# Performance work log

Hardware: AMD Instinct MI355X
Metric: run time of the kernel (lower is better)

## Reference

```python
import jax, jax.numpy as jnp
import numpy as np

B, N, D, H, M, NN, K = 2, 2048, 256, 8, 2, 2048, 8


def setup_inputs() -> dict:
    key = jax.random.key(0)
    ks = jax.random.split(key, 8)
    s = 0.02
    return {
        "current_points": jax.random.normal(ks[0], (B, N, 3), jnp.float32),
        "current_features": jax.random.normal(ks[1], (B, N, D), jnp.float32),
        "neighbor_points": jax.random.normal(ks[2], (M, B, NN, 3), jnp.float32),
        "neighbor_features": jax.random.normal(ks[3], (M, B, NN, D), jnp.float32),
        "in_proj_w": jax.random.normal(ks[4], (3 * D, D), jnp.float32) * s,
        "in_proj_b": jnp.zeros((3 * D,), jnp.float32),
        "out_proj_w": jax.random.normal(ks[5], (D, D), jnp.float32) * s,
        "out_proj_b": jnp.zeros((D,), jnp.float32),
        "spatial_w": jax.random.normal(ks[6], (D, 3), jnp.float32) * s,
        "spatial_b": jnp.zeros((D,), jnp.float32),
    }


def _knn_edge_features(points, features, k):
    # points [b,n,3], features [b,n,d] -> edge features [b,n,d]
    sq = jnp.sum(points * points, axis=-1)                       # [b,n]
    d2 = sq[:, :, None] + sq[:, None, :] - 2.0 * jnp.einsum('bnc,bmc->bnm', points, points)
    _, idx = jax.lax.top_k(-d2, k)                               # k nearest (incl. self), [b,n,k]
    b_idx = jnp.arange(points.shape[0])[:, None, None]
    nbr = features[b_idx, idx]                                   # gather neighbor feats [b,n,k,d]
    return features - jnp.mean(nbr, axis=2)


def _mha(q, kv, in_w, in_b, out_w, out_b, h):
    # torch nn.MultiheadAttention (batch_first) cross-attention
    d = q.shape[-1]
    dh = d // h
    wq, wk, wv = jnp.split(in_w, 3, axis=0)
    bq, bk, bv = jnp.split(in_b, 3, axis=0)
    qp = q @ wq.T + bq                                           # [b,Lq,d]
    kp = kv @ wk.T + bk                                          # [b,Lk,d]
    vp = kv @ wv.T + bv

    def heads(x):
        b, l, _ = x.shape
        return x.reshape(b, l, h, dh).transpose(0, 2, 1, 3)      # [b,h,l,dh]

    qh, kh, vh = heads(qp), heads(kp), heads(vp)
    scores = jnp.einsum('bhqd,bhkd->bhqk', qh, kh) / np.sqrt(dh).astype(np.float32)
    attn = jax.nn.softmax(scores, axis=-1)
    o = jnp.einsum('bhqk,bhkd->bhqd', attn, vh)
    b, _, lq, _ = o.shape
    o = o.transpose(0, 2, 1, 3).reshape(b, lq, d)
    return o @ out_w.T + out_b


def reference(current_points, current_features, neighbor_points, neighbor_features,
              in_proj_w, in_proj_b, out_proj_w, out_proj_b, spatial_w, spatial_b):
    cur_edge = _knn_edge_features(current_points, current_features, K)       # [B,N,D]
    nbr_edge = jax.vmap(lambda p, f: _knn_edge_features(p, f, K))(neighbor_points, neighbor_features)  # [M,B,NN,D]
    all_nbr = jnp.transpose(nbr_edge, (1, 0, 2, 3)).reshape(B, M * NN, D)    # cat along seq dim
    aligned = _mha(cur_edge, all_nbr, in_proj_w, in_proj_b, out_proj_w, out_proj_b, H)
    spatial = current_points @ spatial_w.T + spatial_b                       # [B,N,D]
    return aligned + spatial
```

## Files before the change

kernel.cpp:

```cpp
#include <hip/hip_runtime.h>
#include <hip/hip_bf16.h>

typedef __bf16 bf16_t;
typedef __attribute__((ext_vector_type(8))) __bf16 bf16x8;
typedef __attribute__((ext_vector_type(4))) __bf16 bf16x4;
typedef __attribute__((ext_vector_type(4))) float f32x4;


__global__ __launch_bounds__(256) void wconv_kernel(const float* __restrict__ w_in,
                                                    const float* __restrict__ w_out,
                                                    bf16_t* __restrict__ w_in_b,
                                                    bf16_t* __restrict__ w_out_b) {
    int i = blockIdx.x * 256 + threadIdx.x;
    if (i < 768 * 256) w_in_b[i] = (bf16_t)w_in[i];
    if (i < 256 * 256) w_out_b[i] = (bf16_t)w_out[i];
}

__global__ __launch_bounds__(1024) void knn_kernel(const float* __restrict__ cur_pts,
                                                   const float* __restrict__ nbr_pts,
                                                   int* __restrict__ idx_out) {
    int p = blockIdx.y;
    const float* pts = (p < 2) ? (cur_pts + (size_t)p * 2048 * 3)
                               : (nbr_pts + (size_t)(p - 2) * 2048 * 3);

    __shared__ __align__(16) float4 spts[2048];

    int tid = threadIdx.x;
    for (int i = tid; i < 2048; i += 1024) {
        float x = pts[i * 3 + 0], y = pts[i * 3 + 1], z = pts[i * 3 + 2];
        float sq = __fadd_rn(__fadd_rn(__fmul_rn(x, x), __fmul_rn(y, y)), __fmul_rn(z, z));
        spts[i] = make_float4(x, y, z, sq);
    }
    __syncthreads();

    int wave = tid >> 6, lane = tid & 63;
    int q = blockIdx.x * 16 + wave;
    float4 qp4 = spts[q];

    float dist[8];
    int di[8];
#pragma unroll
    for (int r = 0; r < 8; r++) { dist[r] = 3.4e38f; di[r] = 0x7fffffff; }

    for (int t = 0; t < 32; t++) {
        int j = t * 64 + lane;
        float4 pp = spts[j];
        float dot = __fadd_rn(__fadd_rn(__fmul_rn(qp4.x, pp.x), __fmul_rn(qp4.y, pp.y)),
                              __fmul_rn(qp4.z, pp.z));
        float d2 = __fsub_rn(__fadd_rn(qp4.w, pp.w), __fmul_rn(2.0f, dot));
        if (d2 < dist[7]) {
#pragma unroll
            for (int r = 7; r >= 1; --r) {
                bool cm = d2 < dist[r - 1];
                bool cr = d2 < dist[r];
                float nd = cm ? dist[r - 1] : (cr ? d2 : dist[r]);
                int ni = cm ? di[r - 1] : (cr ? j : di[r]);
                dist[r] = nd; di[r] = ni;
            }
            if (d2 < dist[0]) { dist[0] = d2; di[0] = j; }
        }
    }

    int res[8];
#pragma unroll
    for (int r = 0; r < 8; r++) {
        float bd = dist[0];
        int bi = di[0];
#pragma unroll
        for (int m = 1; m < 64; m <<= 1) {
            float od = __shfl_xor(bd, m);
            int oi = __shfl_xor(bi, m);
            if (od < bd || (od == bd && oi < bi)) { bd = od; bi = oi; }
        }
        res[r] = bi;
        bool win = (di[0] == bi);
#pragma unroll
        for (int k = 0; k < 7; k++) {
            dist[k] = win ? dist[k + 1] : dist[k];
            di[k]   = win ? di[k + 1]   : di[k];
        }
        if (win) { dist[7] = 3.4e38f; di[7] = 0x7fffffff; }
    }

    if (lane == 0) {
        int4* o = (int4*)(idx_out + ((size_t)p * 2048 + q) * 8);
        o[0] = make_int4(res[0], res[1], res[2], res[3]);
        o[1] = make_int4(res[4], res[5], res[6], res[7]);
    }
}

__global__ __launch_bounds__(64) void edge_kernel(const float* __restrict__ cur_feat,
                                                  const float* __restrict__ nbr_feat,
                                                  const int* __restrict__ idx_buf,
                                                  bf16_t* __restrict__ cur_edge,
                                                  bf16_t* __restrict__ all_nbr) {
    int blk = blockIdx.x;
    int p = blk >> 11, q = blk & 2047;
    const float* feat;
    bf16_t* outp;
    if (p < 2) {
        feat = cur_feat + (size_t)p * 2048 * 256;
        outp = cur_edge + ((size_t)p * 2048 + q) * 256;
    } else {
        int mb = p - 2;
        int m = mb >> 1, bb = mb & 1;
        feat = nbr_feat + (size_t)mb * 2048 * 256;
        outp = all_nbr + ((size_t)bb * 4096 + m * 2048 + q) * 256;
    }
    const int* idx = idx_buf + ((size_t)p * 2048 + q) * 8;
    int t = threadIdx.x;
    float4 self = ((const float4*)(feat + (size_t)q * 256))[t];
    float sx = 0.f, sy = 0.f, sz = 0.f, sw = 0.f;
#pragma unroll
    for (int r = 0; r < 8; r++) {
        float4 f = ((const float4*)(feat + (size_t)idx[r] * 256))[t];
        sx += f.x; sy += f.y; sz += f.z; sw += f.w;
    }
    bf16x4 v;
    v[0] = (bf16_t)(self.x - sx * 0.125f);
    v[1] = (bf16_t)(self.y - sy * 0.125f);
    v[2] = (bf16_t)(self.z - sz * 0.125f);
    v[3] = (bf16_t)(self.w - sw * 0.125f);
    *(bf16x4*)(outp + 4 * t) = v;
}

__global__ __launch_bounds__(256) void qkv_kernel(const bf16_t* __restrict__ cur_edge,
                                                  const bf16_t* __restrict__ all_nbr,
                                                  const bf16_t* __restrict__ w_in,
                                                  const float* __restrict__ b_in,
                                                  bf16_t* __restrict__ qp,
                                                  bf16_t* __restrict__ kp,
                                                  bf16_t* __restrict__ vpT) {
    int z = blockIdx.z;
    int Mrows = (z == 0) ? 4096 : 8192;
    int m0base = blockIdx.y * 64;
    if (m0base >= Mrows) return;
    const bf16_t* A = (z == 0) ? cur_edge : all_nbr;
    const bf16_t* W = w_in + (size_t)z * 256 * 256;

    int wave = threadIdx.x >> 6, lane = threadIdx.x & 63;
    int wr = wave >> 1, wc = wave & 1;
    int m0 = m0base + wr * 32;
    int n0 = blockIdx.x * 64 + wc * 32;
    int lr = lane & 15, lg = lane >> 4;

    f32x4 acc[2][2] = {};
    for (int kc = 0; kc < 256; kc += 32) {
        bf16x8 a[2], b[2];
#pragma unroll
        for (int i = 0; i < 2; i++)
            a[i] = *(const bf16x8*)(A + (size_t)(m0 + i * 16 + lr) * 256 + kc + lg * 8);
#pragma unroll
        for (int i = 0; i < 2; i++)
            b[i] = *(const bf16x8*)(W + (size_t)(n0 + i * 16 + lr) * 256 + kc + lg * 8);
#pragma unroll
        for (int i = 0; i < 2; i++)
#pragma unroll
            for (int j = 0; j < 2; j++)
                acc[i][j] = __builtin_amdgcn_mfma_f32_16x16x32_bf16(a[i], b[j], acc[i][j], 0, 0, 0);
    }

    const float inv_s = 0.17677669529663687f;
#pragma unroll
    for (int i = 0; i < 2; i++)
#pragma unroll
        for (int j = 0; j < 2; j++)
#pragma unroll
            for (int r = 0; r < 4; r++) {
                int mm = m0 + i * 16 + lg * 4 + r;
                int nn = n0 + j * 16 + lr;
                float v = acc[i][j][r] + b_in[z * 256 + nn];
                if (z == 0) {
                    qp[(size_t)mm * 256 + nn] = (bf16_t)(v * inv_s);
                } else if (z == 1) {
                    kp[(size_t)mm * 256 + nn] = (bf16_t)v;
                } else {
                    int bb = mm >> 12, kv = mm & 4095, h = nn >> 5, dd = nn & 31;
                    vpT[(((size_t)bb * 8 + h) * 32 + dd) * 4096 + kv] = (bf16_t)v;
                }
            }
}

__global__ __launch_bounds__(256) void attn_kernel(const bf16_t* __restrict__ qp,
                                                   const bf16_t* __restrict__ kp,
                                                   const bf16_t* __restrict__ vpT,
                                                   bf16_t* __restrict__ Opart,
                                                   float* __restrict__ Lpart) {
    int bh = blockIdx.y;
    int b = bh >> 3, h = bh & 7;
    int c = blockIdx.z;
    int wave = threadIdx.x >> 6, lane = threadIdx.x & 63;
    int lr = lane & 15, lg = lane >> 4;
    int q0 = blockIdx.x * 128 + wave * 32;

    const bf16_t* Qb = qp + ((size_t)b * 2048 + q0) * 256 + h * 32;
    const bf16_t* Kb = kp + (size_t)b * 4096 * 256 + h * 32;
    const bf16_t* Vb = vpT + ((size_t)b * 8 + h) * 32 * 4096;

    __shared__ __align__(16) bf16_t P_lds[4][2][16][32];

    bf16x8 qfrag[2];
    qfrag[0] = *(const bf16x8*)(Qb + (size_t)lr * 256 + lg * 8);
    qfrag[1] = *(const bf16x8*)(Qb + (size_t)(16 + lr) * 256 + lg * 8);

    f32x4 oacc[2][2] = {};
    float lsum[2][4] = {};
    const f32x4 zf = {0.f, 0.f, 0.f, 0.f};

    int kv_lo = c * 1024, kv_hi = kv_lo + 1024;
    for (int kv0 = kv_lo; kv0 < kv_hi; kv0 += 32) {
        bf16x8 kfrag[2];
        kfrag[0] = *(const bf16x8*)(Kb + (size_t)(kv0 + lr) * 256 + lg * 8);
        kfrag[1] = *(const bf16x8*)(Kb + (size_t)(kv0 + 16 + lr) * 256 + lg * 8);

#pragma unroll
        for (int ms = 0; ms < 2; ms++) {
            f32x4 s0 = __builtin_amdgcn_mfma_f32_16x16x32_bf16(qfrag[ms], kfrag[0], zf, 0, 0, 0);
            f32x4 s1 = __builtin_amdgcn_mfma_f32_16x16x32_bf16(qfrag[ms], kfrag[1], zf, 0, 0, 0);
#pragma unroll
            for (int r = 0; r < 4; r++) {
                float p0 = __expf(s0[r]);
                float p1 = __expf(s1[r]);
                lsum[ms][r] += p0 + p1;
                P_lds[wave][ms][lg * 4 + r][lr] = (bf16_t)p0;
                P_lds[wave][ms][lg * 4 + r][16 + lr] = (bf16_t)p1;
            }
        }

        bf16x8 vfrag[2];
        vfrag[0] = *(const bf16x8*)(Vb + (size_t)lr * 4096 + kv0 + lg * 8);
        vfrag[1] = *(const bf16x8*)(Vb + (size_t)(16 + lr) * 4096 + kv0 + lg * 8);

#pragma unroll
        for (int ms = 0; ms < 2; ms++) {
            bf16x8 pf = *(const bf16x8*)(&P_lds[wave][ms][lr][lg * 8]);
            oacc[ms][0] = __builtin_amdgcn_mfma_f32_16x16x32_bf16(pf, vfrag[0], oacc[ms][0], 0, 0, 0);
            oacc[ms][1] = __builtin_amdgcn_mfma_f32_16x16x32_bf16(pf, vfrag[1], oacc[ms][1], 0, 0, 0);
        }
    }

#pragma unroll
    for (int ms = 0; ms < 2; ms++)
#pragma unroll
        for (int r = 0; r < 4; r++) {
            float s = lsum[ms][r];
            s += __shfl_xor(s, 1);
            s += __shfl_xor(s, 2);
            s += __shfl_xor(s, 4);
            s += __shfl_xor(s, 8);
            lsum[ms][r] = s;
        }

#pragma unroll
    for (int ms = 0; ms < 2; ms++)
#pragma unroll
        for (int r = 0; r < 4; r++) {
            int qq = q0 + ms * 16 + lg * 4 + r;
            if (lr == 0)
                Lpart[(((size_t)c * 2 + b) * 8 + h) * 2048 + qq] = lsum[ms][r];
#pragma unroll
            for (int ds = 0; ds < 2; ds++) {
                int dd = h * 32 + ds * 16 + lr;
                Opart[(((size_t)c * 2 + b) * 2048 + qq) * 256 + dd] = (bf16_t)oacc[ms][ds][r];
            }
        }
}

__global__ __launch_bounds__(256) void attn_combine(const bf16_t* __restrict__ Opart,
                                                    const float* __restrict__ Lpart,
                                                    bf16_t* __restrict__ o_buf) {
    int t = blockIdx.x * 256 + threadIdx.x;
    int row = t >> 5;
    int c8 = (t & 31) * 8;
    int b = row >> 11, q = row & 2047, h = c8 >> 5;

    float acc[8] = {};
    float l = 0.f;
#pragma unroll
    for (int c = 0; c < 4; c++) {
        bf16x8 v = *(const bf16x8*)(Opart + (((size_t)c * 2 + b) * 2048 + q) * 256 + c8);
#pragma unroll
        for (int j = 0; j < 8; j++) acc[j] += (float)v[j];
        l += Lpart[(((size_t)c * 2 + b) * 8 + h) * 2048 + q];
    }
    float rl = 1.0f / l;
    bf16x8 o;
#pragma unroll
    for (int j = 0; j < 8; j++) o[j] = (bf16_t)(acc[j] * rl);
    *(bf16x8*)(o_buf + (size_t)row * 256 + c8) = o;
}

__global__ __launch_bounds__(256) void outproj_kernel(const bf16_t* __restrict__ o_buf,
                                                      const bf16_t* __restrict__ w_out,
                                                      const float* __restrict__ b_out,
                                                      const float* __restrict__ cur_pts,
                                                      const float* __restrict__ sw,
                                                      const float* __restrict__ sb,
                                                      float* __restrict__ out) {
    int wave = threadIdx.x >> 6, lane = threadIdx.x & 63;
    int wr = wave >> 1, wc = wave & 1;
    int m0 = blockIdx.y * 64 + wr * 32;
    int n0 = blockIdx.x * 64 + wc * 32;
    int lr = lane & 15, lg = lane >> 4;

    f32x4 acc[2][2] = {};
    for (int kc = 0; kc < 256; kc += 32) {
        bf16x8 a[2], b[2];
#pragma unroll
        for (int i = 0; i < 2; i++)
            a[i] = *(const bf16x8*)(o_buf + (size_t)(m0 + i * 16 + lr) * 256 + kc + lg * 8);
#pragma unroll
        for (int i = 0; i < 2; i++)
            b[i] = *(const bf16x8*)(w_out + (size_t)(n0 + i * 16 + lr) * 256 + kc + lg * 8);
#pragma unroll
        for (int i = 0; i < 2; i++)
#pragma unroll
            for (int j = 0; j < 2; j++)
                acc[i][j] = __builtin_amdgcn_mfma_f32_16x16x32_bf16(a[i], b[j], acc[i][j], 0, 0, 0);
    }

#pragma unroll
    for (int i = 0; i < 2; i++)
#pragma unroll
        for (int j = 0; j < 2; j++)
#pragma unroll
            for (int r = 0; r < 4; r++) {
                int mm = m0 + i * 16 + lg * 4 + r;
                int nn = n0 + j * 16 + lr;
                const float* pp = cur_pts + (size_t)mm * 3;
                float sp = pp[0] * sw[nn * 3 + 0] + pp[1] * sw[nn * 3 + 1] + pp[2] * sw[nn * 3 + 2] + sb[nn];
                out[(size_t)mm * 256 + nn] = acc[i][j][r] + b_out[nn] + sp;
            }
}

extern "C" void kernel_launch(void* const* d_in, const int* in_sizes, int n_in,
                              void* d_out, int out_size, void* d_ws, size_t ws_size,
                              hipStream_t stream) {
    const float* cur_pts  = (const float*)d_in[0];
    const float* cur_feat = (const float*)d_in[1];
    const float* nbr_pts  = (const float*)d_in[2];
    const float* nbr_feat = (const float*)d_in[3];
    const float* in_w     = (const float*)d_in[4];
    const float* in_b     = (const float*)d_in[5];
    const float* out_w    = (const float*)d_in[6];
    const float* out_b    = (const float*)d_in[7];
    const float* sw       = (const float*)d_in[8];
    const float* sb       = (const float*)d_in[9];

    char* ws = (char*)d_ws;
    bf16_t* w_in_b  = (bf16_t*)(ws + 0);
    bf16_t* w_out_b = (bf16_t*)(ws + 393216);
    int*    idx_buf = (int*)(ws + 524288);
    bf16_t* cur_edge = (bf16_t*)(ws + 917504);
    bf16_t* all_nbr  = (bf16_t*)(ws + 3014656);
    bf16_t* qp  = (bf16_t*)(ws + 7208960);
    bf16_t* kp  = (bf16_t*)(ws + 9306112);
    bf16_t* vpT = (bf16_t*)(ws + 13500416);
    bf16_t* o_buf = (bf16_t*)(ws + 17694720);
    bf16_t* Opart = (bf16_t*)(ws + 19791872);
    float*  Lpart = (float*)(ws + 28180480);
    float* outp = (float*)d_out;

    wconv_kernel<<<dim3(768), dim3(256), 0, stream>>>(in_w, out_w, w_in_b, w_out_b);
    knn_kernel<<<dim3(128, 6), dim3(1024), 0, stream>>>(cur_pts, nbr_pts, idx_buf);
    edge_kernel<<<dim3(12288), dim3(64), 0, stream>>>(cur_feat, nbr_feat, idx_buf, cur_edge, all_nbr);
    qkv_kernel<<<dim3(4, 128, 3), dim3(256), 0, stream>>>(cur_edge, all_nbr, w_in_b, in_b, qp, kp, vpT);
    attn_kernel<<<dim3(16, 16, 4), dim3(256), 0, stream>>>(qp, kp, vpT, Opart, Lpart);
    attn_combine<<<dim3(512), dim3(256), 0, stream>>>(Opart, Lpart, o_buf);
    outproj_kernel<<<dim3(4, 64), dim3(256), 0, stream>>>(o_buf, w_out_b, out_b, cur_pts, sw, sb, outp);
}
```

Baseline: 221.3 us.

## Stage K/V tiles cooperatively in LDS and halve queries per wave in attention

The attention kernel now has each wave handle 16 query rows instead of 32, and the grid is doubled to cover them. K and V tiles for each 32-key step are loaded once per block by the four waves, each wave loading one quarter, and held in shared memory with a register prefetch of the next tile. Previously every wave fetched its own K/V fragments from global memory. The change cuts redundant global loads and raises occupancy (launch bounds 256,8), but adds two block barriers per iteration and halves MFMA work per wave, so latency hiding depends on having many resident blocks.

```diff
diff --git a/kernel.cpp b/kernel.cpp
--- a/kernel.cpp
+++ b/kernel.cpp
@@ -181,89 +181,101 @@
             }
 }
 
-__global__ __launch_bounds__(256) void attn_kernel(const bf16_t* __restrict__ qp,
-                                                   const bf16_t* __restrict__ kp,
-                                                   const bf16_t* __restrict__ vpT,
-                                                   bf16_t* __restrict__ Opart,
-                                                   float* __restrict__ Lpart) {
+__global__ __launch_bounds__(256, 8) void attn_kernel(const bf16_t* __restrict__ qp,
+                                                      const bf16_t* __restrict__ kp,
+                                                      const bf16_t* __restrict__ vpT,
+                                                      bf16_t* __restrict__ Opart,
+                                                      float* __restrict__ Lpart) {
     int bh = blockIdx.y;
     int b = bh >> 3, h = bh & 7;
     int c = blockIdx.z;
     int wave = threadIdx.x >> 6, lane = threadIdx.x & 63;
     int lr = lane & 15, lg = lane >> 4;
-    int q0 = blockIdx.x * 128 + wave * 32;
+    int q0 = blockIdx.x * 64 + wave * 16;
 
     const bf16_t* Qb = qp + ((size_t)b * 2048 + q0) * 256 + h * 32;
     const bf16_t* Kb = kp + (size_t)b * 4096 * 256 + h * 32;
     const bf16_t* Vb = vpT + ((size_t)b * 8 + h) * 32 * 4096;
 
-    __shared__ __align__(16) bf16_t P_lds[4][2][16][32];
-
-    bf16x8 qfrag[2];
-    qfrag[0] = *(const bf16x8*)(Qb + (size_t)lr * 256 + lg * 8);
-    qfrag[1] = *(const bf16x8*)(Qb + (size_t)(16 + lr) * 256 + lg * 8);
-
-    f32x4 oacc[2][2] = {};
-    float lsum[2][4] = {};
+    __shared__ __align__(16) bf16_t KV[2048];
+    __shared__ __align__(16) bf16_t P_lds[4][512];
+    bf16_t* Pw = &P_lds[wave][0];
+
+    bf16x8 qfrag = *(const bf16x8*)(Qb + (size_t)lr * 256 + lg * 8);
+
+    f32x4 oacc[2] = {};
+    float lsum[4] = {};
     const f32x4 zf = {0.f, 0.f, 0.f, 0.f};
 
-    int kv_lo = c * 1024, kv_hi = kv_lo + 1024;
-    for (int kv0 = kv_lo; kv0 < kv_hi; kv0 += 32) {
-        bf16x8 kfrag[2];
-        kfrag[0] = *(const bf16x8*)(Kb + (size_t)(kv0 + lr) * 256 + lg * 8);
-        kfrag[1] = *(const bf16x8*)(Kb + (size_t)(kv0 + 16 + lr) * 256 + lg * 8);
-
-#pragma unroll
-        for (int ms = 0; ms < 2; ms++) {
-            f32x4 s0 = __builtin_amdgcn_mfma_f32_16x16x32_bf16(qfrag[ms], kfrag[0], zf, 0, 0, 0);
-            f32x4 s1 = __builtin_amdgcn_mfma_f32_16x16x32_bf16(qfrag[ms], kfrag[1], zf, 0, 0, 0);
-#pragma unroll
-            for (int r = 0; r < 4; r++) {
-                float p0 = __expf(s0[r]);
-                float p1 = __expf(s1[r]);
-                lsum[ms][r] += p0 + p1;
-                P_lds[wave][ms][lg * 4 + r][lr] = (bf16_t)p0;
-                P_lds[wave][ms][lg * 4 + r][16 + lr] = (bf16_t)p1;
-            }
-        }
-
-        bf16x8 vfrag[2];
-        vfrag[0] = *(const bf16x8*)(Vb + (size_t)lr * 4096 + kv0 + lg * 8);
-        vfrag[1] = *(const bf16x8*)(Vb + (size_t)(16 + lr) * 4096 + kv0 + lg * 8);
-
-#pragma unroll
-        for (int ms = 0; ms < 2; ms++) {
-            bf16x8 pf = *(const bf16x8*)(&P_lds[wave][ms][lr][lg * 8]);
-            oacc[ms][0] = __builtin_amdgcn_mfma_f32_16x16x32_bf16(pf, vfrag[0], oacc[ms][0], 0, 0, 0);
-            oacc[ms][1] = __builtin_amdgcn_mfma_f32_16x16x32_bf16(pf, vfrag[1], oacc[ms][1], 0, 0, 0);
-        }
-    }
-
-#pragma unroll
-    for (int ms = 0; ms < 2; ms++)
+    int kv_lo = c * 1024;
+
+    int role = wave;
+    int tlr = lr, tlg = lg;
+    const bf16_t* gsrc;
+    size_t gstep;
+    if (role < 2) {
+        gsrc = Kb + (size_t)(kv_lo + role * 16 + tlr) * 256 + tlg * 8;
+        gstep = 32 * 256;
+    } else {
+        gsrc = Vb + (size_t)((role - 2) * 16 + tlr) * 4096 + kv_lo + tlg * 8;
+        gstep = 32;
+    }
+    bf16_t* stage_dst = &KV[(size_t)threadIdx.x * 8];
+
+    bf16x8 g = *(const bf16x8*)gsrc;
+    gsrc += gstep;
+
+    for (int t = 0; t < 32; t++) {
+        *(bf16x8*)stage_dst = g;
+        if (t + 1 < 32) {
+            g = *(const bf16x8*)gsrc;
+            gsrc += gstep;
+        }
+        __syncthreads();
+
+        bf16x8 kf0 = *(const bf16x8*)(KV + (size_t)lane * 8);
+        bf16x8 kf1 = *(const bf16x8*)(KV + 512 + (size_t)lane * 8);
+        bf16x8 vf0 = *(const bf16x8*)(KV + 1024 + (size_t)lane * 8);
+        bf16x8 vf1 = *(const bf16x8*)(KV + 1536 + (size_t)lane * 8);
+
+        f32x4 s0 = __builtin_amdgcn_mfma_f32_16x16x32_bf16(qfrag, kf0, zf, 0, 0, 0);
+        f32x4 s1 = __builtin_amdgcn_mfma_f32_16x16x32_bf16(qfrag, kf1, zf, 0, 0, 0);
 #pragma unroll
         for (int r = 0; r < 4; r++) {
-            float s = lsum[ms][r];
-            s += __shfl_xor(s, 1);
-            s += __shfl_xor(s, 2);
-            s += __shfl_xor(s, 4);
-            s += __shfl_xor(s, 8);
-            lsum[ms][r] = s;
-        }
-
-#pragma unroll
-    for (int ms = 0; ms < 2; ms++)
-#pragma unroll
-        for (int r = 0; r < 4; r++) {
-            int qq = q0 + ms * 16 + lg * 4 + r;
-            if (lr == 0)
-                Lpart[(((size_t)c * 2 + b) * 8 + h) * 2048 + qq] = lsum[ms][r];
-#pragma unroll
-            for (int ds = 0; ds < 2; ds++) {
-                int dd = h * 32 + ds * 16 + lr;
-                Opart[(((size_t)c * 2 + b) * 2048 + qq) * 256 + dd] = (bf16_t)oacc[ms][ds][r];
-            }
-        }
+            float p0 = __expf(s0[r]);
+            float p1 = __expf(s1[r]);
+            lsum[r] += p0 + p1;
+            Pw[((lr >> 3) * 128) + (lg * 4 + r) * 8 + (lr & 7)] = (bf16_t)p0;
+            Pw[((2 + (lr >> 3)) * 128) + (lg * 4 + r) * 8 + (lr & 7)] = (bf16_t)p1;
+        }
+        bf16x8 pf = *(const bf16x8*)(Pw + (size_t)lane * 8);
+        oacc[0] = __builtin_amdgcn_mfma_f32_16x16x32_bf16(pf, vf0, oacc[0], 0, 0, 0);
+        oacc[1] = __builtin_amdgcn_mfma_f32_16x16x32_bf16(pf, vf1, oacc[1], 0, 0, 0);
+
+        __syncthreads();
+    }
+
+#pragma unroll
+    for (int r = 0; r < 4; r++) {
+        float s = lsum[r];
+        s += __shfl_xor(s, 1);
+        s += __shfl_xor(s, 2);
+        s += __shfl_xor(s, 4);
+        s += __shfl_xor(s, 8);
+        lsum[r] = s;
+    }
+
+#pragma unroll
+    for (int r = 0; r < 4; r++) {
+        int qq = q0 + lg * 4 + r;
+        if (lr == 0)
+            Lpart[(((size_t)c * 2 + b) * 8 + h) * 2048 + qq] = lsum[r];
+#pragma unroll
+        for (int ds = 0; ds < 2; ds++) {
+            int dd = h * 32 + ds * 16 + lr;
+            Opart[(((size_t)c * 2 + b) * 2048 + qq) * 256 + dd] = (bf16_t)oacc[ds][r];
+        }
+    }
 }
 
 __global__ __launch_bounds__(256) void attn_combine(const bf16_t* __restrict__ Opart,
@@ -365,7 +377,7 @@
     knn_kernel<<<dim3(128, 6), dim3(1024), 0, stream>>>(cur_pts, nbr_pts, idx_buf);
     edge_kernel<<<dim3(12288), dim3(64), 0, stream>>>(cur_feat, nbr_feat, idx_buf, cur_edge, all_nbr);
     qkv_kernel<<<dim3(4, 128, 3), dim3(256), 0, stream>>>(cur_edge, all_nbr, w_in_b, in_b, qp, kp, vpT);
-    attn_kernel<<<dim3(16, 16, 4), dim3(256), 0, stream>>>(qp, kp, vpT, Opart, Lpart);
+    attn_kernel<<<dim3(32, 16, 4), dim3(256), 0, stream>>>(qp, kp, vpT, Opart, Lpart);
     attn_combine<<<dim3(512), dim3(256), 0, stream>>>(Opart, Lpart, o_buf);
     outproj_kernel<<<dim3(4, 64), dim3(256), 0, stream>>>(o_buf, w_out_b, out_b, cur_pts, sw, sb, outp);
 }
```

New measurement: 202.6 us. 8.5% less time.

## Transpose V via LDS, swizzle P tile, remap attention blocks for XCD locality

Applied to the files above, without the earlier changes.

The QKV projection now writes V row-major, and a new transpose kernel builds the per-head V^T through shared memory. This replaces the scattered strided stores in the QKV epilogue. The attention kernel swaps MFMA operands so each lane holds consecutive kv scores, packs P into 8-byte LDS stores with an XOR swizzle, and reduces row sums with fewer shuffles. It also loads K and V fragments together up front, flattens the grid with a mapping that puts the same head and chunk on one XCD, and sets occupancy launch bounds. The cost is one extra kernel launch and an extra V round trip through memory, with the vp buffer aliased over the Opart region.

```diff
diff --git a/kernel.cpp b/kernel.cpp
--- a/kernel.cpp
+++ b/kernel.cpp
@@ -6,6 +6,12 @@
 typedef __attribute__((ext_vector_type(4))) __bf16 bf16x4;
 typedef __attribute__((ext_vector_type(4))) float f32x4;
 
+
+static __device__ __forceinline__ unsigned pk2(float x, float y) {
+    unsigned short ux = __builtin_bit_cast(unsigned short, (bf16_t)x);
+    unsigned short uy = __builtin_bit_cast(unsigned short, (bf16_t)y);
+    return (unsigned)ux | ((unsigned)uy << 16);
+}
 
 __global__ __launch_bounds__(256) void wconv_kernel(const float* __restrict__ w_in,
                                                     const float* __restrict__ w_out,
@@ -130,7 +136,7 @@
                                                   const float* __restrict__ b_in,
                                                   bf16_t* __restrict__ qp,
                                                   bf16_t* __restrict__ kp,
-                                                  bf16_t* __restrict__ vpT) {
+                                                  bf16_t* __restrict__ vp) {
     int z = blockIdx.z;
     int Mrows = (z == 0) ? 4096 : 8192;
     int m0base = blockIdx.y * 64;
@@ -175,89 +181,133 @@
                 } else if (z == 1) {
                     kp[(size_t)mm * 256 + nn] = (bf16_t)v;
                 } else {
-                    int bb = mm >> 12, kv = mm & 4095, h = nn >> 5, dd = nn & 31;
-                    vpT[(((size_t)bb * 8 + h) * 32 + dd) * 4096 + kv] = (bf16_t)v;
+                    vp[(size_t)mm * 256 + nn] = (bf16_t)v;
                 }
             }
 }
 
-__global__ __launch_bounds__(256) void attn_kernel(const bf16_t* __restrict__ qp,
-                                                   const bf16_t* __restrict__ kp,
-                                                   const bf16_t* __restrict__ vpT,
-                                                   bf16_t* __restrict__ Opart,
-                                                   float* __restrict__ Lpart) {
+__global__ __launch_bounds__(256) void vt_kernel(const bf16_t* __restrict__ vp,
+                                                 bf16_t* __restrict__ vpT) {
+    int kc = blockIdx.x;
     int bh = blockIdx.y;
     int b = bh >> 3, h = bh & 7;
-    int c = blockIdx.z;
+    __shared__ bf16_t tile[64][34];
+    int tid = threadIdx.x;
+
+    const bf16_t* src = vp + ((size_t)b * 4096 + kc * 64) * 256 + h * 32;
+    int dd0 = (tid & 7) * 4, kvr = tid >> 3;
+#pragma unroll
+    for (int it = 0; it < 2; it++) {
+        int kv = it * 32 + kvr;
+        bf16x4 v = *(const bf16x4*)(src + (size_t)kv * 256 + dd0);
+#pragma unroll
+        for (int j = 0; j < 4; j++) tile[kv][dd0 + j] = v[j];
+    }
+    __syncthreads();
+
+    bf16_t* dst = vpT + (((size_t)b * 8 + h) * 32) * 4096 + kc * 64;
+    int kv0 = (tid & 15) * 4, ddr0 = tid >> 4;
+#pragma unroll
+    for (int it = 0; it < 2; it++) {
+        int dd = it * 16 + ddr0;
+        bf16x4 v;
+#pragma unroll
+        for (int j = 0; j < 4; j++) v[j] = tile[kv0 + j][dd];
+        *(bf16x4*)(dst + (size_t)dd * 4096 + kv0) = v;
+    }
+}
+
+__global__ __launch_bounds__(256, 4) void attn_kernel(const bf16_t* __restrict__ qp,
+                                                      const bf16_t* __restrict__ kp,
+                                                      const bf16_t* __restrict__ vpT,
+                                                      bf16_t* __restrict__ Opart,
+                                                      float* __restrict__ Lpart) {
+    int d = blockIdx.x;
+    int xcd = d & 7, j = d >> 3;
+    int xb = j & 15;
+    int g = xcd + 8 * (j >> 4);
+    int bh = g & 15, c = g >> 4;
+    int b = bh >> 3, h = bh & 7;
+
     int wave = threadIdx.x >> 6, lane = threadIdx.x & 63;
     int lr = lane & 15, lg = lane >> 4;
-    int q0 = blockIdx.x * 128 + wave * 32;
+    int q0 = xb * 128 + wave * 32;
 
     const bf16_t* Qb = qp + ((size_t)b * 2048 + q0) * 256 + h * 32;
     const bf16_t* Kb = kp + (size_t)b * 4096 * 256 + h * 32;
     const bf16_t* Vb = vpT + ((size_t)b * 8 + h) * 32 * 4096;
 
-    __shared__ __align__(16) bf16_t P_lds[4][2][16][32];
-
-    bf16x8 qfrag[2];
-    qfrag[0] = *(const bf16x8*)(Qb + (size_t)lr * 256 + lg * 8);
-    qfrag[1] = *(const bf16x8*)(Qb + (size_t)(16 + lr) * 256 + lg * 8);
+    __shared__ __align__(16) char P_lds[4][2048];
+    char* Pw = &P_lds[wave][0];
+
+    bf16x8 qf[2];
+    qf[0] = *(const bf16x8*)(Qb + (size_t)lr * 256 + lg * 8);
+    qf[1] = *(const bf16x8*)(Qb + (size_t)(16 + lr) * 256 + lg * 8);
 
     f32x4 oacc[2][2] = {};
-    float lsum[2][4] = {};
+    float lsum[2] = {0.f, 0.f};
     const f32x4 zf = {0.f, 0.f, 0.f, 0.f};
 
-    int kv_lo = c * 1024, kv_hi = kv_lo + 1024;
-    for (int kv0 = kv_lo; kv0 < kv_hi; kv0 += 32) {
-        bf16x8 kfrag[2];
-        kfrag[0] = *(const bf16x8*)(Kb + (size_t)(kv0 + lr) * 256 + lg * 8);
-        kfrag[1] = *(const bf16x8*)(Kb + (size_t)(kv0 + 16 + lr) * 256 + lg * 8);
+    int wb[2][2], rb[2];
+#pragma unroll
+    for (int ms = 0; ms < 2; ms++) {
+        rb[ms] = (ms * 16 + lr) * 64 + ((lg ^ (lr & 3)) << 4);
+#pragma unroll
+        for (int kvs = 0; kvs < 2; kvs++)
+            wb[ms][kvs] = (ms * 16 + lr) * 64 +
+                          (((kvs * 2 + (lg >> 1)) ^ (lr & 3)) << 4) + ((lg & 1) << 3);
+    }
+
+    int kv_lo = c * 1024;
+    for (int t = 0; t < 32; t++) {
+        int kv0 = kv_lo + t * 32;
+        bf16x8 kf0 = *(const bf16x8*)(Kb + (size_t)(kv0 + lr) * 256 + lg * 8);
+        bf16x8 kf1 = *(const bf16x8*)(Kb + (size_t)(kv0 + 16 + lr) * 256 + lg * 8);
+        bf16x8 vf0 = *(const bf16x8*)(Vb + (size_t)lr * 4096 + kv0 + lg * 8);
+        bf16x8 vf1 = *(const bf16x8*)(Vb + (size_t)(16 + lr) * 4096 + kv0 + lg * 8);
 
 #pragma unroll
         for (int ms = 0; ms < 2; ms++) {
-            f32x4 s0 = __builtin_amdgcn_mfma_f32_16x16x32_bf16(qfrag[ms], kfrag[0], zf, 0, 0, 0);
-            f32x4 s1 = __builtin_amdgcn_mfma_f32_16x16x32_bf16(qfrag[ms], kfrag[1], zf, 0, 0, 0);
-#pragma unroll
-            for (int r = 0; r < 4; r++) {
-                float p0 = __expf(s0[r]);
-                float p1 = __expf(s1[r]);
-                lsum[ms][r] += p0 + p1;
-                P_lds[wave][ms][lg * 4 + r][lr] = (bf16_t)p0;
-                P_lds[wave][ms][lg * 4 + r][16 + lr] = (bf16_t)p1;
-            }
-        }
-
-        bf16x8 vfrag[2];
-        vfrag[0] = *(const bf16x8*)(Vb + (size_t)lr * 4096 + kv0 + lg * 8);
-        vfrag[1] = *(const bf16x8*)(Vb + (size_t)(16 + lr) * 4096 + kv0 + lg * 8);
+            f32x4 s0 = __builtin_amdgcn_mfma_f32_16x16x32_bf16(kf0, qf[ms], zf, 0, 0, 0);
+            f32x4 s1 = __builtin_amdgcn_mfma_f32_16x16x32_bf16(kf1, qf[ms], zf, 0, 0, 0);
+            float p00 = __expf(s0[0]), p01 = __expf(s0[1]);
+            float p02 = __expf(s0[2]), p03 = __expf(s0[3]);
+            float p10 = __expf(s1[0]), p11 = __expf(s1[1]);
+            float p12 = __expf(s1[2]), p13 = __expf(s1[3]);
+            lsum[ms] += (p00 + p01) + (p02 + p03) + (p10 + p11) + (p12 + p13);
+            uint2 w0, w1;
+            w0.x = pk2(p00, p01); w0.y = pk2(p02, p03);
+            w1.x = pk2(p10, p11); w1.y = pk2(p12, p13);
+            *(uint2*)(Pw + wb[ms][0]) = w0;
+            *(uint2*)(Pw + wb[ms][1]) = w1;
+        }
 
 #pragma unroll
         for (int ms = 0; ms < 2; ms++) {
-            bf16x8 pf = *(const bf16x8*)(&P_lds[wave][ms][lr][lg * 8]);
-            oacc[ms][0] = __builtin_amdgcn_mfma_f32_16x16x32_bf16(pf, vfrag[0], oacc[ms][0], 0, 0, 0);
-            oacc[ms][1] = __builtin_amdgcn_mfma_f32_16x16x32_bf16(pf, vfrag[1], oacc[ms][1], 0, 0, 0);
-        }
-    }
-
-#pragma unroll
-    for (int ms = 0; ms < 2; ms++)
-#pragma unroll
-        for (int r = 0; r < 4; r++) {
-            float s = lsum[ms][r];
-            s += __shfl_xor(s, 1);
-            s += __shfl_xor(s, 2);
-            s += __shfl_xor(s, 4);
-            s += __shfl_xor(s, 8);
-            lsum[ms][r] = s;
-        }
+            bf16x8 pf = *(const bf16x8*)(Pw + rb[ms]);
+            oacc[ms][0] = __builtin_amdgcn_mfma_f32_16x16x32_bf16(pf, vf0, oacc[ms][0], 0, 0, 0);
+            oacc[ms][1] = __builtin_amdgcn_mfma_f32_16x16x32_bf16(pf, vf1, oacc[ms][1], 0, 0, 0);
+        }
+    }
+
+#pragma unroll
+    for (int ms = 0; ms < 2; ms++) {
+        float s = lsum[ms];
+        s += __shfl_xor(s, 16);
+        s += __shfl_xor(s, 32);
+        lsum[ms] = s;
+    }
+
+    if (lg == 0) {
+        Lpart[(((size_t)c * 2 + b) * 8 + h) * 2048 + q0 + lr] = lsum[0];
+        Lpart[(((size_t)c * 2 + b) * 8 + h) * 2048 + q0 + 16 + lr] = lsum[1];
+    }
 
 #pragma unroll
     for (int ms = 0; ms < 2; ms++)
 #pragma unroll
         for (int r = 0; r < 4; r++) {
             int qq = q0 + ms * 16 + lg * 4 + r;
-            if (lr == 0)
-                Lpart[(((size_t)c * 2 + b) * 8 + h) * 2048 + qq] = lsum[ms][r];
 #pragma unroll
             for (int ds = 0; ds < 2; ds++) {
                 int dd = h * 32 + ds * 16 + lr;
@@ -359,13 +409,15 @@
     bf16_t* o_buf = (bf16_t*)(ws + 17694720);
     bf16_t* Opart = (bf16_t*)(ws + 19791872);
     float*  Lpart = (float*)(ws + 28180480);
+    bf16_t* vp = (bf16_t*)(ws + 19791872);
     float* outp = (float*)d_out;
 
     wconv_kernel<<<dim3(768), dim3(256), 0, stream>>>(in_w, out_w, w_in_b, w_out_b);
     knn_kernel<<<dim3(128, 6), dim3(1024), 0, stream>>>(cur_pts, nbr_pts, idx_buf);
     edge_kernel<<<dim3(12288), dim3(64), 0, stream>>>(cur_feat, nbr_feat, idx_buf, cur_edge, all_nbr);
-    qkv_kernel<<<dim3(4, 128, 3), dim3(256), 0, stream>>>(cur_edge, all_nbr, w_in_b, in_b, qp, kp, vpT);
-    attn_kernel<<<dim3(16, 16, 4), dim3(256), 0, stream>>>(qp, kp, vpT, Opart, Lpart);
+    qkv_kernel<<<dim3(4, 128, 3), dim3(256), 0, stream>>>(cur_edge, all_nbr, w_in_b, in_b, qp, kp, vp);
+    vt_kernel<<<dim3(64, 16), dim3(256), 0, stream>>>(vp, vpT);
+    attn_kernel<<<dim3(1024), dim3(256), 0, stream>>>(qp, kp, vpT, Opart, Lpart);
     attn_combine<<<dim3(512), dim3(256), 0, stream>>>(Opart, Lpart, o_buf);
     outproj_kernel<<<dim3(4, 64), dim3(256), 0, stream>>>(o_buf, w_out_b, out_b, cur_pts, sw, sb, outp);
 }
```

After: 222.0 us. Within noise of the previous version (+0.3%).
